# Kernel optimization log

Measured on AMD Instinct MI355X. Metric: run time of the kernel, lower is better.

Reference implementation:

```python
import jax, jax.numpy as jnp
import numpy as np

# hyperparameters (from init_kwargs)
NEG_POS_RATIO = 3
THRESHOLD = 0.5
VAR0, VAR1 = 0.1, 0.2
NUM_FRAMES = 8
NUM_CLASSES = 2


def _point_form(priors):
    # center form (cx,cy,w,h) -> corner form (x1,y1,x2,y2)
    return jnp.concatenate([priors[:, :2] - priors[:, 2:] * 0.5,
                            priors[:, :2] + priors[:, 2:] * 0.5], axis=1)


def _iou(truths, priors_pt):
    # truths [O,4] corner form, priors_pt [A,4] corner form -> [O,A]
    lt = jnp.maximum(truths[:, None, :2], priors_pt[None, :, :2])
    rb = jnp.minimum(truths[:, None, 2:], priors_pt[None, :, 2:])
    wh = jnp.clip(rb - lt, 0.0)
    inter = wh[..., 0] * wh[..., 1]
    area_t = ((truths[:, 2] - truths[:, 0]) * (truths[:, 3] - truths[:, 1]))[:, None]
    area_p = ((priors_pt[:, 2] - priors_pt[:, 0]) * (priors_pt[:, 3] - priors_pt[:, 1]))[None, :]
    return inter / (area_t + area_p - inter)


def _match(truths, labels, priors):
    # SSD match + encode for one (batch, frame)
    O = truths.shape[0]
    ov = _iou(truths, _point_form(priors))          # [O, A]
    best_prior_idx = jnp.argmax(ov, axis=1)          # [O] best anchor per truth
    best_truth_ov = jnp.max(ov, axis=0)              # [A]
    best_truth_idx = jnp.argmax(ov, axis=0)          # [A]
    # ensure every truth keeps its best anchor
    best_truth_ov = best_truth_ov.at[best_prior_idx].set(2.0)
    best_truth_idx = best_truth_idx.at[best_prior_idx].set(jnp.arange(O))
    matched = truths[best_truth_idx]                 # [A, 4]
    conf = labels[best_truth_idx].astype(jnp.int32) + 1
    conf = jnp.where(best_truth_ov < THRESHOLD, 0, conf)
    # encode offsets
    g_cxcy = ((matched[:, :2] + matched[:, 2:]) * 0.5 - priors[:, :2]) / (VAR0 * priors[:, 2:])
    g_wh = jnp.log((matched[:, 2:] - matched[:, :2]) / priors[:, 2:]) / VAR1
    return jnp.concatenate([g_cxcy, g_wh], axis=1), conf


def setup_inputs() -> dict:
    key = jax.random.key(0)
    k1, k2, k3, k4, k5, k6 = jax.random.split(key, 6)
    B, F_, A, O, C = 32, NUM_FRAMES, 8732, 32, NUM_CLASSES
    # anchors in center form, inside unit square
    a_cxcy = jax.random.uniform(k1, (A, 2), minval=0.05, maxval=0.95)
    a_wh = jax.random.uniform(k2, (A, 2), minval=0.02, maxval=0.30)
    anchors = jnp.concatenate([a_cxcy, a_wh], axis=1).astype(jnp.float32)
    # ground truth boxes (corner form, valid) + label 0 (single fg class)
    t_cxcy = jax.random.uniform(k3, (B, F_, O, 2), minval=0.15, maxval=0.85)
    t_wh = jax.random.uniform(k4, (B, F_, O, 2), minval=0.05, maxval=0.25)
    boxes = jnp.concatenate([t_cxcy - t_wh * 0.5, t_cxcy + t_wh * 0.5], axis=-1)
    boxes = jnp.clip(boxes, 1e-3, 1.0)
    labels = jnp.zeros((B, F_, O, 1), dtype=jnp.float32)
    targets = jnp.concatenate([boxes, labels], axis=-1).astype(jnp.float32)
    loc_data = jax.random.normal(k5, (B, F_ * A, 4), dtype=jnp.float32)
    conf_data = jax.random.normal(k6, (B, F_ * A, C), dtype=jnp.float32)
    return {"loc_data": loc_data, "conf_data": conf_data, "anchors": anchors, "targets": targets}


def reference(loc_data, conf_data, anchors, targets):
    B = loc_data.shape[0]
    F_ = NUM_FRAMES
    A = anchors.shape[0]
    truths = targets[..., :4].reshape(B * F_, -1, 4)
    labels = targets[..., 4].reshape(B * F_, -1)
    loc_t, conf_t = jax.vmap(_match, in_axes=(0, 0, None))(truths, labels, anchors)  # [BF,A,4], [BF,A]

    pos = conf_t > 0                                   # [BF, A]
    pos3 = pos.reshape(B, F_, A)

    # localization smooth-L1 loss over positives (sum)
    d = loc_data.reshape(B * F_, A, 4) - loc_t
    ad = jnp.abs(d)
    sl1 = jnp.where(ad < 1.0, 0.5 * d * d, ad - 0.5)
    loss_l = jnp.sum(sl1 * pos[..., None].astype(sl1.dtype))

    # per-anchor confidence loss for hard-negative mining
    flat_conf = conf_data.reshape(-1, NUM_CLASSES)
    lse = jax.nn.logsumexp(flat_conf, axis=1)
    gathered = jnp.take_along_axis(flat_conf, conf_t.reshape(-1, 1), axis=1)[:, 0]
    lc = (lse - gathered).reshape(B, F_, A)
    lc = jnp.where(pos3, 0.0, lc)

    # hard negative mining: double argsort rank per frame
    loss_idx = jnp.argsort(-lc, axis=2)
    idx_rank = jnp.argsort(loss_idx, axis=2)
    num_pos = jnp.sum(pos3.astype(jnp.int32), axis=2, keepdims=True)
    num_neg = jnp.minimum(NEG_POS_RATIO * num_pos, A - 1)
    neg3 = idx_rank < num_neg
    sel = pos3 | neg3

    # BCE between argmax class prediction and conf_t (as in source)
    pred = jnp.argmax(conf_data.reshape(B, F_, A, NUM_CLASSES), axis=3).astype(conf_data.dtype)
    tgt = conf_t.reshape(B, F_, A).astype(conf_data.dtype)
    logp = jnp.maximum(jnp.log(jnp.clip(pred, 1e-12, 1.0)), -100.0)
    log1mp = jnp.maximum(jnp.log(jnp.clip(1.0 - pred, 1e-12, 1.0)), -100.0)
    bce = -(tgt * logp + (1.0 - tgt) * log1mp)
    loss_c = jnp.sum(bce * sel.astype(bce.dtype))
    return loss_l, loss_c
```

## Files before the change

### kernel.cpp

```cpp
#include <hip/hip_runtime.h>
#include <math.h>

#define A_NUM 8732
#define O_NUM 32
#define NEGPOS 3
#define NTHR 256
#define NWAVE 4
#define ASPLIT 12
#define APB 728
#define K_ANCH 3
#define LOGEPS_F (-27.631021115928547f)

__device__ __forceinline__ unsigned int rotu(unsigned int v) {
    return (unsigned int)__builtin_amdgcn_update_dpp((int)v, (int)v, 0x121, 0xf, 0xf, false);
}
__device__ __forceinline__ float rotf(float v) {
    return __int_as_float((int)rotu((unsigned int)__float_as_int(v)));
}

__device__ __forceinline__ unsigned int iou_hi(float tx1, float ty1, float tx2, float ty2, float ta,
                                               float px1, float py1, float px2, float py2, float ap) {
    float w = __saturatef(fminf(tx2, px2) - fmaxf(tx1, px1));
    float h = __saturatef(fminf(ty2, py2) - fmaxf(ty1, py1));
    float inter = w * h;
    float uni = (ta + ap) - inter;
    float iou = inter * __builtin_amdgcn_rcpf(uni);
    return __float_as_uint(iou) & 0xFFFFC000u;
}

__device__ __forceinline__ float sl1_sum(float4 t, float4 pr, float4 ld) {
    float gx = ((t.x + t.z) * 0.5f - pr.x) / (0.1f * pr.z);
    float gy = ((t.y + t.w) * 0.5f - pr.y) / (0.1f * pr.w);
    float gw = logf((t.z - t.x) / pr.z) / 0.2f;
    float gh = logf((t.w - t.y) / pr.w) / 0.2f;
    float d0 = ld.x - gx, d1 = ld.y - gy, d2 = ld.z - gw, d3 = ld.w - gh;
    float a0 = fabsf(d0), a1 = fabsf(d1), a2 = fabsf(d2), a3 = fabsf(d3);
    float s0 = (a0 < 1.0f) ? 0.5f * d0 * d0 : a0 - 0.5f;
    float s1 = (a1 < 1.0f) ? 0.5f * d1 * d1 : a1 - 0.5f;
    float s2 = (a2 < 1.0f) ? 0.5f * d2 * d2 : a2 - 0.5f;
    float s3 = (a3 < 1.0f) ? 0.5f * d3 * d3 : a3 - 0.5f;
    return s0 + s1 + s2 + s3;
}

__device__ __forceinline__ float bce_pos(int pred, float tgt) {
    float logp   = (pred == 0) ? LOGEPS_F : 0.0f;
    float log1mp = (pred == 1) ? LOGEPS_F : 0.0f;
    return -(tgt * logp + (1.0f - tgt) * log1mp);
}

__global__ __launch_bounds__(NTHR) void mfbl_k1(
    const float* __restrict__ loc_data, const float* __restrict__ conf_data,
    const float* __restrict__ anchors, const float* __restrict__ targets,
    unsigned int* __restrict__ g_tred, float4* __restrict__ g_part)
{
    const int split = blockIdx.x;
    const int frame = blockIdx.y;
    const int a_lo = split * APB;
    const int nA = min(a_lo + APB, A_NUM) - a_lo;
    const int tid = threadIdx.x;
    const int lane = tid & 63;
    const int wid  = tid >> 6;
    const int r = lane >> 4;
    const int i = lane & 15;

    __shared__ float4 s_tc[O_NUM];
    __shared__ float  s_lab[O_NUM];
    __shared__ unsigned int s_tred[O_NUM][NWAVE];
    __shared__ float s_r[4][NWAVE];

    if (tid < O_NUM) {
        const float* t = targets + ((size_t)frame * O_NUM + tid) * 5;
        s_tc[tid] = make_float4(t[0], t[1], t[2], t[3]);
        s_lab[tid] = t[4];
    }

    float px1[K_ANCH], py1[K_ANCH], px2[K_ANCH], py2[K_ANCH], ap[K_ANCH];
    unsigned int bestA[K_ANCH], aT[K_ANCH];
    float2 cd[K_ANCH];
#pragma unroll
    for (int k = 0; k < K_ANCH; ++k) {
        int idx = tid + k * NTHR;
        int ic = min(idx, nA - 1);
        float4 pr = *(const float4*)(anchors + (size_t)(a_lo + ic) * 4);
        float hw = pr.z * 0.5f, hh = pr.w * 0.5f;
        px1[k] = pr.x - hw; py1[k] = pr.y - hh;
        px2[k] = pr.x + hw; py2[k] = pr.y + hh;
        ap[k] = (px2[k] - px1[k]) * (py2[k] - py1[k]);
        bestA[k] = 0u;
        aT[k] = 16383u - (unsigned int)(a_lo + idx);
        cd[k] = make_float2(0.0f, 0.0f);
        if (idx < nA)
            cd[k] = *(const float2*)(conf_data + ((size_t)frame * A_NUM + a_lo + idx) * 2);
    }
    __syncthreads();

    unsigned int tbp[2];
    for (int p = 0; p < 2; ++p) {
        const int t0 = (((r + p) & 1) << 4) | i;
        float4 tc = s_tc[t0];
        float ta = (tc.z - tc.x) * (tc.w - tc.y);
        unsigned int oc = (unsigned int)(31 - t0);
        unsigned int tb = 0u;
#pragma unroll
        for (int s = 0; s < 16; ++s) {
#pragma unroll
            for (int k = 0; k < K_ANCH; ++k) {
                unsigned int hi = iou_hi(tc.x, tc.y, tc.z, tc.w, ta,
                                         px1[k], py1[k], px2[k], py2[k], ap[k]);
                bestA[k] = max(bestA[k], hi | oc);
                tb = max(tb, hi | aT[k]);
            }
            tc.x = rotf(tc.x); tc.y = rotf(tc.y);
            tc.z = rotf(tc.z); tc.w = rotf(tc.w);
            ta = rotf(ta); oc = rotu(oc); tb = rotu(tb);
        }
        tbp[p] = tb;
    }

    unsigned int v = max(tbp[0], (unsigned int)__shfl_xor((int)tbp[1], 16));
    v = max(v, (unsigned int)__shfl_xor((int)v, 32));
    if (lane < O_NUM) s_tred[lane][wid] = v;
    __syncthreads();
    if (tid < O_NUM) {
        unsigned int k = s_tred[tid][0];
        for (int w = 1; w < NWAVE; ++w) k = max(k, s_tred[tid][w]);
        atomicMax(&g_tred[(size_t)frame * O_NUM + tid], k);
    }

    float l_sum = 0.0f, cpos = 0.0f, np_cnt = 0.0f, m_cnt = 0.0f;
#pragma unroll
    for (int k = 0; k < K_ANCH; ++k) {
        int idx = tid + k * NTHR;
        if (idx < nA) {
            unsigned int key = bestA[k];
            int bo = 31 - (int)(key & 31u);
            unsigned int hi = key & 0xFFFFC000u;
            int a = a_lo + idx;
            int pred = (cd[k].y > cd[k].x) ? 1 : 0;
            int cv = (hi >= 0x3F000000u) ? (int)s_lab[bo] + 1 : 0;
            if (cv > 0) {
                np_cnt += 1.0f;
                float4 pr = *(const float4*)(anchors + (size_t)a * 4);
                float4 ld = *(const float4*)(loc_data + ((size_t)frame * A_NUM + a) * 4);
                l_sum += sl1_sum(s_tc[bo], pr, ld);
                cpos += bce_pos(pred, (float)cv);
            } else {
                m_cnt += (float)pred;
            }
        }
    }
    for (int s = 32; s > 0; s >>= 1) {
        l_sum  += __shfl_down(l_sum, s);
        cpos   += __shfl_down(cpos, s);
        np_cnt += __shfl_down(np_cnt, s);
        m_cnt  += __shfl_down(m_cnt, s);
    }
    if (lane == 0) { s_r[0][wid] = l_sum; s_r[1][wid] = cpos; s_r[2][wid] = np_cnt; s_r[3][wid] = m_cnt; }
    __syncthreads();
    if (tid == 0) {
        float L = 0, C = 0, NP = 0, M = 0;
        for (int w = 0; w < NWAVE; ++w) { L += s_r[0][w]; C += s_r[1][w]; NP += s_r[2][w]; M += s_r[3][w]; }
        g_part[frame * ASPLIT + split] = make_float4(L, C, NP, M);
    }
}

__global__ __launch_bounds__(64) void mfbl_k2(
    const float* __restrict__ loc_data, const float* __restrict__ conf_data,
    const float* __restrict__ anchors, const float* __restrict__ targets,
    const unsigned int* __restrict__ g_tred, const float4* __restrict__ g_part,
    float* __restrict__ ws_l, float* __restrict__ ws_c)
{
    const int frame = blockIdx.x;
    const int tid = threadIdx.x;

    __shared__ float4 s_tc[O_NUM];
    __shared__ float s_ta[O_NUM], s_lab[O_NUM];
    __shared__ int s_bp[O_NUM];

    if (tid < O_NUM) {
        const float* t = targets + ((size_t)frame * O_NUM + tid) * 5;
        float x1 = t[0], y1 = t[1], x2 = t[2], y2 = t[3];
        s_tc[tid] = make_float4(x1, y1, x2, y2);
        s_ta[tid] = (x2 - x1) * (y2 - y1);
        s_lab[tid] = t[4];
        unsigned int k = g_tred[(size_t)frame * O_NUM + tid];
        s_bp[tid] = 16383 - (int)(k & 16383u);
    }
    __syncthreads();

    float dL = 0.0f, dC = 0.0f, dNP = 0.0f, dM = 0.0f;
    if (tid < O_NUM) {
        int a = s_bp[tid];
        bool owner = true;
        for (int o2 = tid + 1; o2 < O_NUM; ++o2)
            if (s_bp[o2] == a) owner = false;
        if (owner) {
            float4 pr = *(const float4*)(anchors + (size_t)a * 4);
            float hw = pr.z * 0.5f, hh = pr.w * 0.5f;
            float px1 = pr.x - hw, py1 = pr.y - hh;
            float px2 = pr.x + hw, py2 = pr.y + hh;
            float apn = (px2 - px1) * (py2 - py1);
            unsigned int bk = 0u;
            for (int o2 = 0; o2 < O_NUM; ++o2) {
                float4 t = s_tc[o2];
                unsigned int hi = iou_hi(t.x, t.y, t.z, t.w, s_ta[o2], px1, py1, px2, py2, apn);
                bk = max(bk, hi | (unsigned int)(31 - o2));
            }
            int old_o = 31 - (int)(bk & 31u);
            unsigned int old_hi = bk & 0xFFFFC000u;
            int old_cv = (old_hi >= 0x3F000000u) ? (int)s_lab[old_o] + 1 : 0;
            const float2 cdv = *(const float2*)(conf_data + ((size_t)frame * A_NUM + a) * 2);
            int pred = (cdv.y > cdv.x) ? 1 : 0;
            float4 ld = *(const float4*)(loc_data + ((size_t)frame * A_NUM + a) * 4);
            int new_cv = (int)s_lab[tid] + 1;
            dL = sl1_sum(s_tc[tid], pr, ld);
            dC = bce_pos(pred, (float)new_cv);
            dNP = 1.0f;
            if (old_cv > 0) {
                dL -= sl1_sum(s_tc[old_o], pr, ld);
                dC -= bce_pos(pred, (float)old_cv);
                dNP -= 1.0f;
            } else {
                dM -= (float)pred;
            }
        }
    }
    for (int s = 32; s > 0; s >>= 1) {
        dL += __shfl_down(dL, s);
        dC += __shfl_down(dC, s);
        dNP += __shfl_down(dNP, s);
        dM += __shfl_down(dM, s);
    }
    if (tid == 0) {
        float L = 0, C = 0, NP = 0, M = 0;
        for (int s = 0; s < ASPLIT; ++s) {
            float4 p = g_part[frame * ASPLIT + s];
            L += p.x; C += p.y; NP += p.z; M += p.w;
        }
        L += dL; C += dC; NP += dNP; M += dM;
        int np = (int)NP, m = (int)M;
        int num_neg = min(NEGPOS * np, A_NUM - 1);
        int nsel = min(num_neg, m);
        ws_l[frame] = L;
        ws_c[frame] = C + 27.631021115928547f * (float)nsel;
    }
}

__global__ void mfbl_k3(const float* __restrict__ ws_l, const float* __restrict__ ws_c,
                        float* __restrict__ out, int n) {
    int tid = threadIdx.x;
    float a = (tid < n) ? ws_l[tid] : 0.0f;
    float b = (tid < n) ? ws_c[tid] : 0.0f;
    for (int s = 32; s > 0; s >>= 1) {
        a += __shfl_down(a, s);
        b += __shfl_down(b, s);
    }
    __shared__ float sa[4], sb[4];
    int lane = tid & 63, wid = tid >> 6;
    if (lane == 0) { sa[wid] = a; sb[wid] = b; }
    __syncthreads();
    if (tid == 0) {
        float A = 0.0f, B = 0.0f;
        for (int w = 0; w < 4; ++w) { A += sa[w]; B += sb[w]; }
        out[0] = A;
        out[1] = B;
    }
}

extern "C" void kernel_launch(void* const* d_in, const int* in_sizes, int n_in,
                              void* d_out, int out_size, void* d_ws, size_t ws_size,
                              hipStream_t stream) {
    const float* loc     = (const float*)d_in[0];
    const float* conf    = (const float*)d_in[1];
    const float* anchors = (const float*)d_in[2];
    const float* targets = (const float*)d_in[3];
    float* out = (float*)d_out;
    (void)ws_size;

    const int BF = in_sizes[3] / (O_NUM * 5);
    const int NBLK = BF * ASPLIT;

    unsigned int* g_tred = (unsigned int*)d_ws;
    float4* g_part = (float4*)((char*)d_ws + (size_t)BF * O_NUM * 4);
    float* ws_l = (float*)((char*)g_part + (size_t)NBLK * 16);
    float* ws_c = ws_l + BF;

    hipMemsetAsync(g_tred, 0, (size_t)BF * O_NUM * 4, stream);
    mfbl_k1<<<dim3(ASPLIT, BF), NTHR, 0, stream>>>(loc, conf, anchors, targets, g_tred, g_part);
    mfbl_k2<<<BF, 64, 0, stream>>>(loc, conf, anchors, targets, g_tred, g_part, ws_l, ws_c);
    mfbl_k3<<<1, 256, 0, stream>>>(ws_l, ws_c, out, BF);
}
```

Measured before the change: 80.81 us.

## Use larger blocks covering two frames and batch four frames per k2 block

The matching kernel now launches 1024-thread blocks that each cover about a third of the anchors. Each block loops over two frames, so the anchor corner coordinates are loaded and converted once and reused for both frames. Conf data is now loaded inside the per-frame loop. The finalize kernel packs four frames per 256-thread block, one wave per frame, instead of one 64-thread block per frame. The grid becomes much coarser (384 blocks), which risks poor load balance across CUs and lower occupancy. It also assumes the frame count divides by 2 and by 4.

After: 123.3 us. +52.5%, slower.

```diff
diff --git a/kernel.cpp b/kernel.cpp
--- a/kernel.cpp
+++ b/kernel.cpp
@@ -4,11 +4,12 @@
 #define A_NUM 8732
 #define O_NUM 32
 #define NEGPOS 3
-#define NTHR 256
-#define NWAVE 4
-#define ASPLIT 12
-#define APB 728
+#define NTHR 1024
+#define NWAVE 16
+#define ASPLIT 3
+#define APB 2911
 #define K_ANCH 3
+#define FPB 2
 #define LOGEPS_F (-27.631021115928547f)
 
 __device__ __forceinline__ unsigned int rotu(unsigned int v) {
@@ -54,7 +55,7 @@
     unsigned int* __restrict__ g_tred, float4* __restrict__ g_part)
 {
     const int split = blockIdx.x;
-    const int frame = blockIdx.y;
+    const int frame0 = blockIdx.y * FPB;
     const int a_lo = split * APB;
     const int nA = min(a_lo + APB, A_NUM) - a_lo;
     const int tid = threadIdx.x;
@@ -68,15 +69,8 @@
     __shared__ unsigned int s_tred[O_NUM][NWAVE];
     __shared__ float s_r[4][NWAVE];
 
-    if (tid < O_NUM) {
-        const float* t = targets + ((size_t)frame * O_NUM + tid) * 5;
-        s_tc[tid] = make_float4(t[0], t[1], t[2], t[3]);
-        s_lab[tid] = t[4];
-    }
-
     float px1[K_ANCH], py1[K_ANCH], px2[K_ANCH], py2[K_ANCH], ap[K_ANCH];
-    unsigned int bestA[K_ANCH], aT[K_ANCH];
-    float2 cd[K_ANCH];
+    unsigned int aT[K_ANCH];
 #pragma unroll
     for (int k = 0; k < K_ANCH; ++k) {
         int idx = tid + k * NTHR;
@@ -86,114 +80,125 @@
         px1[k] = pr.x - hw; py1[k] = pr.y - hh;
         px2[k] = pr.x + hw; py2[k] = pr.y + hh;
         ap[k] = (px2[k] - px1[k]) * (py2[k] - py1[k]);
-        bestA[k] = 0u;
         aT[k] = 16383u - (unsigned int)(a_lo + idx);
-        cd[k] = make_float2(0.0f, 0.0f);
-        if (idx < nA)
-            cd[k] = *(const float2*)(conf_data + ((size_t)frame * A_NUM + a_lo + idx) * 2);
-    }
-    __syncthreads();
-
-    unsigned int tbp[2];
-    for (int p = 0; p < 2; ++p) {
-        const int t0 = (((r + p) & 1) << 4) | i;
-        float4 tc = s_tc[t0];
-        float ta = (tc.z - tc.x) * (tc.w - tc.y);
-        unsigned int oc = (unsigned int)(31 - t0);
-        unsigned int tb = 0u;
-#pragma unroll
-        for (int s = 0; s < 16; ++s) {
-#pragma unroll
-            for (int k = 0; k < K_ANCH; ++k) {
-                unsigned int hi = iou_hi(tc.x, tc.y, tc.z, tc.w, ta,
-                                         px1[k], py1[k], px2[k], py2[k], ap[k]);
-                bestA[k] = max(bestA[k], hi | oc);
-                tb = max(tb, hi | aT[k]);
-            }
-            tc.x = rotf(tc.x); tc.y = rotf(tc.y);
-            tc.z = rotf(tc.z); tc.w = rotf(tc.w);
-            ta = rotf(ta); oc = rotu(oc); tb = rotu(tb);
-        }
-        tbp[p] = tb;
-    }
-
-    unsigned int v = max(tbp[0], (unsigned int)__shfl_xor((int)tbp[1], 16));
-    v = max(v, (unsigned int)__shfl_xor((int)v, 32));
-    if (lane < O_NUM) s_tred[lane][wid] = v;
-    __syncthreads();
-    if (tid < O_NUM) {
-        unsigned int k = s_tred[tid][0];
-        for (int w = 1; w < NWAVE; ++w) k = max(k, s_tred[tid][w]);
-        atomicMax(&g_tred[(size_t)frame * O_NUM + tid], k);
-    }
-
-    float l_sum = 0.0f, cpos = 0.0f, np_cnt = 0.0f, m_cnt = 0.0f;
-#pragma unroll
-    for (int k = 0; k < K_ANCH; ++k) {
-        int idx = tid + k * NTHR;
-        if (idx < nA) {
-            unsigned int key = bestA[k];
-            int bo = 31 - (int)(key & 31u);
-            unsigned int hi = key & 0xFFFFC000u;
-            int a = a_lo + idx;
-            int pred = (cd[k].y > cd[k].x) ? 1 : 0;
-            int cv = (hi >= 0x3F000000u) ? (int)s_lab[bo] + 1 : 0;
-            if (cv > 0) {
-                np_cnt += 1.0f;
-                float4 pr = *(const float4*)(anchors + (size_t)a * 4);
-                float4 ld = *(const float4*)(loc_data + ((size_t)frame * A_NUM + a) * 4);
-                l_sum += sl1_sum(s_tc[bo], pr, ld);
-                cpos += bce_pos(pred, (float)cv);
-            } else {
-                m_cnt += (float)pred;
-            }
-        }
-    }
-    for (int s = 32; s > 0; s >>= 1) {
-        l_sum  += __shfl_down(l_sum, s);
-        cpos   += __shfl_down(cpos, s);
-        np_cnt += __shfl_down(np_cnt, s);
-        m_cnt  += __shfl_down(m_cnt, s);
-    }
-    if (lane == 0) { s_r[0][wid] = l_sum; s_r[1][wid] = cpos; s_r[2][wid] = np_cnt; s_r[3][wid] = m_cnt; }
-    __syncthreads();
-    if (tid == 0) {
-        float L = 0, C = 0, NP = 0, M = 0;
-        for (int w = 0; w < NWAVE; ++w) { L += s_r[0][w]; C += s_r[1][w]; NP += s_r[2][w]; M += s_r[3][w]; }
-        g_part[frame * ASPLIT + split] = make_float4(L, C, NP, M);
-    }
-}
-
-__global__ __launch_bounds__(64) void mfbl_k2(
+    }
+
+    for (int f = 0; f < FPB; ++f) {
+        const int frame = frame0 + f;
+        __syncthreads();
+        if (tid < O_NUM) {
+            const float* t = targets + ((size_t)frame * O_NUM + tid) * 5;
+            s_tc[tid] = make_float4(t[0], t[1], t[2], t[3]);
+            s_lab[tid] = t[4];
+        }
+        __syncthreads();
+
+        unsigned int bestA[K_ANCH];
+#pragma unroll
+        for (int k = 0; k < K_ANCH; ++k) bestA[k] = 0u;
+        unsigned int tbp[2];
+        for (int p = 0; p < 2; ++p) {
+            const int t0 = (((r + p) & 1) << 4) | i;
+            float4 tc = s_tc[t0];
+            float ta = (tc.z - tc.x) * (tc.w - tc.y);
+            unsigned int oc = (unsigned int)(31 - t0);
+            unsigned int tb = 0u;
+#pragma unroll
+            for (int s = 0; s < 16; ++s) {
+#pragma unroll
+                for (int k = 0; k < K_ANCH; ++k) {
+                    unsigned int hi = iou_hi(tc.x, tc.y, tc.z, tc.w, ta,
+                                             px1[k], py1[k], px2[k], py2[k], ap[k]);
+                    bestA[k] = max(bestA[k], hi | oc);
+                    tb = max(tb, hi | aT[k]);
+                }
+                tc.x = rotf(tc.x); tc.y = rotf(tc.y);
+                tc.z = rotf(tc.z); tc.w = rotf(tc.w);
+                ta = rotf(ta); oc = rotu(oc); tb = rotu(tb);
+            }
+            tbp[p] = tb;
+        }
+
+        unsigned int v = max(tbp[0], (unsigned int)__shfl_xor((int)tbp[1], 16));
+        v = max(v, (unsigned int)__shfl_xor((int)v, 32));
+        if (lane < O_NUM) s_tred[lane][wid] = v;
+        __syncthreads();
+        if (tid < O_NUM) {
+            unsigned int k = s_tred[tid][0];
+            for (int w = 1; w < NWAVE; ++w) k = max(k, s_tred[tid][w]);
+            atomicMax(&g_tred[(size_t)frame * O_NUM + tid], k);
+        }
+
+        float l_sum = 0.0f, cpos = 0.0f, np_cnt = 0.0f, m_cnt = 0.0f;
+#pragma unroll
+        for (int k = 0; k < K_ANCH; ++k) {
+            int idx = tid + k * NTHR;
+            if (idx < nA) {
+                unsigned int key = bestA[k];
+                int bo = 31 - (int)(key & 31u);
+                unsigned int hi = key & 0xFFFFC000u;
+                int a = a_lo + idx;
+                const float2 cdv = *(const float2*)(conf_data + ((size_t)frame * A_NUM + a) * 2);
+                int pred = (cdv.y > cdv.x) ? 1 : 0;
+                int cv = (hi >= 0x3F000000u) ? (int)s_lab[bo] + 1 : 0;
+                if (cv > 0) {
+                    np_cnt += 1.0f;
+                    float4 pr = *(const float4*)(anchors + (size_t)a * 4);
+                    float4 ld = *(const float4*)(loc_data + ((size_t)frame * A_NUM + a) * 4);
+                    l_sum += sl1_sum(s_tc[bo], pr, ld);
+                    cpos += bce_pos(pred, (float)cv);
+                } else {
+                    m_cnt += (float)pred;
+                }
+            }
+        }
+        for (int s = 32; s > 0; s >>= 1) {
+            l_sum  += __shfl_down(l_sum, s);
+            cpos   += __shfl_down(cpos, s);
+            np_cnt += __shfl_down(np_cnt, s);
+            m_cnt  += __shfl_down(m_cnt, s);
+        }
+        if (lane == 0) { s_r[0][wid] = l_sum; s_r[1][wid] = cpos; s_r[2][wid] = np_cnt; s_r[3][wid] = m_cnt; }
+        __syncthreads();
+        if (tid == 0) {
+            float L = 0, C = 0, NP = 0, M = 0;
+            for (int w = 0; w < NWAVE; ++w) { L += s_r[0][w]; C += s_r[1][w]; NP += s_r[2][w]; M += s_r[3][w]; }
+            g_part[frame * ASPLIT + split] = make_float4(L, C, NP, M);
+        }
+    }
+}
+
+__global__ __launch_bounds__(256) void mfbl_k2(
     const float* __restrict__ loc_data, const float* __restrict__ conf_data,
     const float* __restrict__ anchors, const float* __restrict__ targets,
     const unsigned int* __restrict__ g_tred, const float4* __restrict__ g_part,
     float* __restrict__ ws_l, float* __restrict__ ws_c)
 {
-    const int frame = blockIdx.x;
-    const int tid = threadIdx.x;
-
-    __shared__ float4 s_tc[O_NUM];
-    __shared__ float s_ta[O_NUM], s_lab[O_NUM];
-    __shared__ int s_bp[O_NUM];
-
-    if (tid < O_NUM) {
-        const float* t = targets + ((size_t)frame * O_NUM + tid) * 5;
+    const int lane = threadIdx.x & 63;
+    const int wid  = threadIdx.x >> 6;
+    const int frame = blockIdx.x * 4 + wid;
+
+    __shared__ float4 s_tc[4][O_NUM];
+    __shared__ float s_ta[4][O_NUM], s_lab[4][O_NUM];
+    __shared__ int s_bp[4][O_NUM];
+
+    if (lane < O_NUM) {
+        const float* t = targets + ((size_t)frame * O_NUM + lane) * 5;
         float x1 = t[0], y1 = t[1], x2 = t[2], y2 = t[3];
-        s_tc[tid] = make_float4(x1, y1, x2, y2);
-        s_ta[tid] = (x2 - x1) * (y2 - y1);
-        s_lab[tid] = t[4];
-        unsigned int k = g_tred[(size_t)frame * O_NUM + tid];
-        s_bp[tid] = 16383 - (int)(k & 16383u);
+        s_tc[wid][lane] = make_float4(x1, y1, x2, y2);
+        s_ta[wid][lane] = (x2 - x1) * (y2 - y1);
+        s_lab[wid][lane] = t[4];
+        unsigned int k = g_tred[(size_t)frame * O_NUM + lane];
+        s_bp[wid][lane] = 16383 - (int)(k & 16383u);
     }
     __syncthreads();
 
     float dL = 0.0f, dC = 0.0f, dNP = 0.0f, dM = 0.0f;
-    if (tid < O_NUM) {
-        int a = s_bp[tid];
+    if (lane < O_NUM) {
+        int a = s_bp[wid][lane];
         bool owner = true;
-        for (int o2 = tid + 1; o2 < O_NUM; ++o2)
-            if (s_bp[o2] == a) owner = false;
+        for (int o2 = lane + 1; o2 < O_NUM; ++o2)
+            if (s_bp[wid][o2] == a) owner = false;
         if (owner) {
             float4 pr = *(const float4*)(anchors + (size_t)a * 4);
             float hw = pr.z * 0.5f, hh = pr.w * 0.5f;
@@ -202,22 +207,22 @@
             float apn = (px2 - px1) * (py2 - py1);
             unsigned int bk = 0u;
             for (int o2 = 0; o2 < O_NUM; ++o2) {
-                float4 t = s_tc[o2];
-                unsigned int hi = iou_hi(t.x, t.y, t.z, t.w, s_ta[o2], px1, py1, px2, py2, apn);
+                float4 t = s_tc[wid][o2];
+                unsigned int hi = iou_hi(t.x, t.y, t.z, t.w, s_ta[wid][o2], px1, py1, px2, py2, apn);
                 bk = max(bk, hi | (unsigned int)(31 - o2));
             }
             int old_o = 31 - (int)(bk & 31u);
             unsigned int old_hi = bk & 0xFFFFC000u;
-            int old_cv = (old_hi >= 0x3F000000u) ? (int)s_lab[old_o] + 1 : 0;
+            int old_cv = (old_hi >= 0x3F000000u) ? (int)s_lab[wid][old_o] + 1 : 0;
             const float2 cdv = *(const float2*)(conf_data + ((size_t)frame * A_NUM + a) * 2);
             int pred = (cdv.y > cdv.x) ? 1 : 0;
             float4 ld = *(const float4*)(loc_data + ((size_t)frame * A_NUM + a) * 4);
-            int new_cv = (int)s_lab[tid] + 1;
-            dL = sl1_sum(s_tc[tid], pr, ld);
+            int new_cv = (int)s_lab[wid][lane] + 1;
+            dL = sl1_sum(s_tc[wid][lane], pr, ld);
             dC = bce_pos(pred, (float)new_cv);
             dNP = 1.0f;
             if (old_cv > 0) {
-                dL -= sl1_sum(s_tc[old_o], pr, ld);
+                dL -= sl1_sum(s_tc[wid][old_o], pr, ld);
                 dC -= bce_pos(pred, (float)old_cv);
                 dNP -= 1.0f;
             } else {
@@ -231,7 +236,7 @@
         dNP += __shfl_down(dNP, s);
         dM += __shfl_down(dM, s);
     }
-    if (tid == 0) {
+    if (lane == 0) {
         float L = 0, C = 0, NP = 0, M = 0;
         for (int s = 0; s < ASPLIT; ++s) {
             float4 p = g_part[frame * ASPLIT + s];
@@ -278,15 +283,14 @@
     (void)ws_size;
 
     const int BF = in_sizes[3] / (O_NUM * 5);
-    const int NBLK = BF * ASPLIT;
 
     unsigned int* g_tred = (unsigned int*)d_ws;
     float4* g_part = (float4*)((char*)d_ws + (size_t)BF * O_NUM * 4);
-    float* ws_l = (float*)((char*)g_part + (size_t)NBLK * 16);
+    float* ws_l = (float*)((char*)g_part + (size_t)BF * ASPLIT * 16);
     float* ws_c = ws_l + BF;
 
     hipMemsetAsync(g_tred, 0, (size_t)BF * O_NUM * 4, stream);
-    mfbl_k1<<<dim3(ASPLIT, BF), NTHR, 0, stream>>>(loc, conf, anchors, targets, g_tred, g_part);
-    mfbl_k2<<<BF, 64, 0, stream>>>(loc, conf, anchors, targets, g_tred, g_part, ws_l, ws_c);
+    mfbl_k1<<<dim3(ASPLIT, BF / FPB), NTHR, 0, stream>>>(loc, conf, anchors, targets, g_tred, g_part);
+    mfbl_k2<<<BF / 4, 256, 0, stream>>>(loc, conf, anchors, targets, g_tred, g_part, ws_l, ws_c);
     mfbl_k3<<<1, 256, 0, stream>>>(ws_l, ws_c, out, BF);
 }
```
